# Kernel optimization log

Hardware: AMD Instinct MI355X
Metric: run time of the kernel (lower is better)

The kernel has to match this reference:

```python
import jax, jax.numpy as jnp
import numpy as np

D = 256          # node_embedding_dim (= GRU hidden per direction)
N = 1024         # number of frame nodes
C = 5            # num_classes
COUNTS = [15, 40, 15]   # num_intervals_per_scale
BINS = [80, 60, 80]     # dist_bins_list
MAX_T = 512      # fixed pad length for per-interval sequences (jit-static)


def _quant(w):
    # int8 per-tensor symmetric fake-quant with straight-through estimator
    s = jnp.maximum(jnp.max(jnp.abs(w)) / 127.0, 1e-8)
    q = jnp.clip(jnp.round(w / s), -128, 127) * s
    return w + jax.lax.stop_gradient(q - w)


def _gru_dir(x, eff, wih, whh, bih, bhh):
    # x: [I, T, D] packed-at-front sequences, eff: [I] valid lengths (>=1)
    # masked scan == torch packed GRU final hidden state
    I, T, _ = x.shape
    H = whh.shape[1]
    valid = jnp.arange(T)[None, :] < eff[:, None]   # [I, T]

    def step(h, inp):
        x_t, v = inp                                # [I,D], [I]
        gi = x_t @ wih.T + bih                      # [I, 3H]
        gh = h @ whh.T + bhh
        ir, iz, inn = jnp.split(gi, 3, axis=1)
        hr, hz, hn = jnp.split(gh, 3, axis=1)
        r = jax.nn.sigmoid(ir + hr)
        z = jax.nn.sigmoid(iz + hz)
        n = jnp.tanh(inn + r * hn)
        h = jnp.where(v[:, None], (1.0 - z) * n + z * h, h)
        return h, None

    h0 = jnp.zeros((I, H), x.dtype)
    hF, _ = jax.lax.scan(step, h0, (jnp.swapaxes(x, 0, 1), valid.T))
    return hF


def _forward(node_embeddings, time_positions, node_pred, audio_len, anchor_intervals,
             gru_wih, gru_whh, gru_bih, gru_bhh, w1, w2,
             w3_s0, w3_s1, w3_s2, sw_s0, ew_s0, sw_s1, ew_s1, sw_s2, ew_s2):
    al = audio_len[0]
    tpos = time_positions[:, 0] * al                     # [N]
    abn = jax.nn.softmax(node_pred, axis=-1)[:, 0]       # abnormal scores [N]
    w3s = [w3_s0, w3_s1, w3_s2]
    sws = [sw_s0, sw_s1, sw_s2]
    ews = [ew_s0, ew_s1, ew_s2]
    offs = np.concatenate([[0], np.cumsum(COUNTS)])
    bounds, confs, clss = [], [], []
    for si in range(3):
        I, b = COUNTS[si], BINS[si]
        anc = anchor_intervals[offs[si]:offs[si + 1]]    # [I, 2]
        starts, ends = anc[:, 0], anc[:, 1]
        # interval membership mask [I, N]
        mask = (tpos[None, :] >= starts[:, None]) & (tpos[None, :] <= ends[:, None])
        # compact valid nodes to the front (stable, preserves node order like x[mask])
        order = jnp.argsort(jnp.logical_not(mask), axis=1, stable=True)[:, :MAX_T]
        msort = jnp.take_along_axis(mask, order, axis=1)
        x_loc = node_embeddings[order] * msort[..., None]   # [I, MAX_T, D]; empty -> zeros row
        eff = jnp.clip(mask.sum(axis=1), 1, MAX_T)          # empty interval behaves as one zero step
        hf = _gru_dir(x_loc, eff, gru_wih[si, 0], gru_whh[si, 0], gru_bih[si, 0], gru_bhh[si, 0])
        # backward direction: reverse each valid prefix
        rev_idx = jnp.clip(eff[:, None] - 1 - jnp.arange(MAX_T)[None, :], 0, MAX_T - 1)
        x_rev = jnp.take_along_axis(x_loc, rev_idx[..., None], axis=1)
        hb = _gru_dir(x_rev, eff, gru_wih[si, 1], gru_whh[si, 1], gru_bih[si, 1], gru_bhh[si, 1])
        # shared feature: [2D | abnormal | center | width | 4 zero pads] = 2D+7
        feat = jnp.concatenate([
            hf, hb,
            abn[:I, None],
            ((starts + ends) * 0.5 / al)[:, None],
            ((ends - starts) / al)[:, None],
            jnp.zeros((I, 4), hf.dtype),
        ], axis=1)
        h = jax.nn.relu(feat @ _quant(w1[si]).T)   # dropout = identity (eval)
        h = jax.nn.relu(h @ _quant(w2[si]).T)
        out = h @ _quant(w3s[si]).T                # [I, 2b+1+(C-1)]
        so = jnp.sum(jax.nn.softmax(out[:, :b], axis=1) * sws[si], axis=1)
        eo = jnp.sum(jax.nn.softmax(out[:, b:2 * b], axis=1) * ews[si], axis=1)
        bounds.append(jnp.stack([jnp.clip(starts + so, 0.0, al), jnp.clip(ends + eo, 0.0, al)], axis=1))
        confs.append(out[:, 2 * b])
        clss.append(out[:, 2 * b + 1:])
    return (jnp.concatenate(bounds, axis=0),   # final_bounds [70, 2]
            jnp.concatenate(confs, axis=0),    # interval_conf_logits [70]
            jnp.concatenate(clss, axis=0))     # interval_cls_logits [70, 4]


def setup_inputs() -> dict:
    key = jax.random.key(0)
    ks = jax.random.split(key, 16)
    inp = {}
    inp["node_embeddings"] = jax.random.normal(ks[0], (N, D), jnp.float32)
    inp["time_positions"] = jax.random.uniform(ks[1], (N, 1), dtype=jnp.float32)
    inp["node_pred"] = jax.random.normal(ks[2], (N, C), jnp.float32)
    inp["audio_len"] = jnp.ones((1,), jnp.float32)
    rng = np.random.default_rng(0)
    widths = [0.05, 0.12, 0.30]
    rows = []
    for c, w in zip(COUNTS, widths):
        s = rng.uniform(0.0, 1.0 - w, size=c).astype(np.float32)
        e = s + rng.uniform(0.5 * w, w, size=c).astype(np.float32)
        rows.append(np.stack([s, e], axis=1))
    inp["anchor_intervals"] = jnp.asarray(np.concatenate(rows, axis=0))
    H = D
    def u(k, shape, fan):
        lim = 1.0 / np.sqrt(fan)
        return jax.random.uniform(k, shape, jnp.float32, -lim, lim)
    # GRU params stacked over [scale, direction]
    inp["gru_wih"] = u(ks[3], (3, 2, 3 * H, D), H)
    inp["gru_whh"] = u(ks[4], (3, 2, 3 * H, H), H)
    inp["gru_bih"] = u(ks[5], (3, 2, 3 * H), H)
    inp["gru_bhh"] = u(ks[6], (3, 2, 3 * H), H)
    F_in = 2 * D + 7
    inp["w1"] = u(ks[7], (3, 256, F_in), F_in)
    inp["w2"] = u(ks[8], (3, 256, 256), 256)
    inp["w3_s0"] = u(ks[9], (2 * BINS[0] + 1 + (C - 1), 256), 256)
    inp["w3_s1"] = u(ks[10], (2 * BINS[1] + 1 + (C - 1), 256), 256)
    inp["w3_s2"] = u(ks[11], (2 * BINS[2] + 1 + (C - 1), 256), 256)
    for i, nb in enumerate(BINS):
        inp[f"sw_s{i}"] = jnp.linspace(-20.0, 20.0, nb, dtype=jnp.float32)
        inp[f"ew_s{i}"] = jnp.linspace(-20.0, 20.0, nb, dtype=jnp.float32)
    return inp


def reference(node_embeddings, time_positions, node_pred, audio_len, anchor_intervals,
              gru_wih, gru_whh, gru_bih, gru_bhh, w1, w2,
              w3_s0, w3_s1, w3_s2, sw_s0, ew_s0, sw_s1, ew_s1, sw_s2, ew_s2):
    return _forward(node_embeddings, time_positions, node_pred, audio_len, anchor_intervals,
                    gru_wih, gru_whh, gru_bih, gru_bhh, w1, w2,
                    w3_s0, w3_s1, w3_s2, sw_s0, ew_s0, sw_s1, ew_s1, sw_s2, ew_s2)
```

## Files before the change

### kernel.cpp

```cpp
#include <hip/hip_runtime.h>
#include <math.h>

#define NN 1024
#define NNP 1025
#define DD 256
#define CC 5
#define G3 768
#define MAXT 512
#define NA 70

typedef _Float16 v8h __attribute__((ext_vector_type(8)));
typedef _Float16 v4h __attribute__((ext_vector_type(4)));
typedef float v4f __attribute__((ext_vector_type(4)));
typedef int v4i __attribute__((ext_vector_type(4)));

#define NF1 (3*16*17*64)
#define NF2 (3*16*8*64)
#define NF3 (3*11*8*64)
#define NFT (NF1+NF2+NF3)

__device__ __forceinline__ float sigf(float x){ return __fdividef(1.f, 1.f + __expf(-x)); }
__device__ __forceinline__ float tanhf_fast(float x){ return 1.f - __fdividef(2.f, __expf(2.f*x) + 1.f); }

__global__ __launch_bounds__(256) void mega_kernel(
    const float* __restrict__ node_pred, const float* __restrict__ tp_in,
    const float* __restrict__ audio_len, const float* __restrict__ anchors,
    const float* __restrict__ whh, const float* __restrict__ wih,
    const float* __restrict__ emb,
    const float* __restrict__ bih, const float* __restrict__ bhh,
    const float* __restrict__ w1, const float* __restrict__ w2,
    const float* __restrict__ w30, const float* __restrict__ w31, const float* __restrict__ w32,
    float* __restrict__ abn, int* __restrict__ order, int* __restrict__ cnteff,
    float* __restrict__ qs, float* __restrict__ cm,
    uint4* __restrict__ whhB8, _Float16* __restrict__ E){
  __shared__ __align__(16) unsigned char smem[16*264*2];
  int b = blockIdx.x, tid = threadIdx.x;
  if (b < 4){
    int i = b*256 + tid;
    float pv[CC]; float m = -1e30f;
    for (int c=0;c<CC;++c){ pv[c]=node_pred[i*CC+c]; m=fmaxf(m,pv[c]); }
    float s=0.f;
    for (int c=0;c<CC;++c) s += expf(pv[c]-m);
    abn[i] = expf(pv[0]-m)/s;
  } else if (b < 74){
    if (tid >= 64) return;
    int a = b-4; int lane = tid;
    float al = audio_len[0];
    float s = anchors[2*a], e = anchors[2*a+1];
    int* ord = order + a*MAXT;
    int cnt = 0;
    for (int base=0; base<NN; base+=64){
      float tp = tp_in[base+lane]*al;
      bool msk = (tp>=s)&&(tp<=e);
      unsigned long long bal = __ballot(msk);
      int off = (int)__popcll(bal & ((1ull<<lane)-1ull));
      if (msk && (cnt+off)<MAXT) ord[cnt+off] = base+lane;
      cnt += (int)__popcll(bal);
    }
    if (lane==0){ int c = cnt<MAXT?cnt:MAXT; cnteff[2*a]=c; cnteff[2*a+1]=(c>0)?c:1; }
  } else if (b < 83){
    int m = b-74;
    const float* p; int n;
    if (m<3){ p = w1 + (size_t)m*256*519; n = 256*519; }
    else if (m<6){ p = w2 + (size_t)(m-3)*256*256; n = 256*256; }
    else { p = (m==6)?w30:((m==7)?w31:w32); n = ((m==7)?125:165)*256; }
    float mx = 0.f;
    for (int i=tid;i<n;i+=256) mx = fmaxf(mx, fabsf(p[i]));
    float* red = (float*)smem;
    red[tid]=mx; __syncthreads();
    for (int sft=128; sft>0; sft>>=1){ if (tid<sft) red[tid]=fmaxf(red[tid],red[tid+sft]); __syncthreads(); }
    if (tid==0) qs[m] = fmaxf(red[0]/127.f, 1e-8f);
  } else if (b < 101){
    int i = (b-83)*256 + tid;
    if (i >= 4608) return;
    int gt = i % 3; int c = (i/3)&255; int sd = i/768;
    int j = gt*256 + c;
    float v = bih[sd*G3+j] + ((gt<2)? bhh[sd*G3+j] : 0.f);
    E[((size_t)(sd*NNP + NN))*1024 + c*4 + gt] = (_Float16)v;
  } else if (b < 149){
    int bb = b-101;
    int sd = bb>>3, w = bb&7;
    float* cm_lds = (float*)smem;
    int lane = tid & 63, wv = tid >> 6;
    for (int it=0; it<24; ++it){
      int lr = it*4 + wv;
      int gt = lr>>5, c = lr&31;
      int j = gt*256 + w*32 + c;
      float4 v = reinterpret_cast<const float4*>(whh + ((size_t)sd*G3 + j)*DD)[lane];
      float mx = fmaxf(fmaxf(fabsf(v.x),fabsf(v.y)), fmaxf(fabsf(v.z),fabsf(v.w)));
      #pragma unroll
      for (int sh=1; sh<64; sh<<=1) mx = fmaxf(mx, __shfl_xor(mx, sh));
      if (lane==0){
        float cmax = fmaxf(mx, 1e-12f);
        cm_lds[lr] = cmax;
        cm[sd*G3 + j] = cmax;
      }
    }
    __syncthreads();
    #pragma unroll
    for (int ee=0; ee<6; ++ee){
      int il = tid*6 + ee;
      int q    = il & 3;
      int nt   = (il>>2) % 6;
      int lane2= il / 24;
      int gt = nt>>1, half = nt&1;
      int j  = gt*256 + w*32 + half*16 + (lane2&15);
      int lr = gt*32  + half*16 + (lane2&15);
      int kbase = 64*q + 16*(lane2>>4);
      float inv = 127.f/cm_lds[lr];
      const float* src = whh + ((size_t)sd*G3 + j)*DD + kbase;
      unsigned int dw[4];
      #pragma unroll
      for (int d2=0; d2<4; ++d2){
        unsigned int acc = 0;
        #pragma unroll
        for (int e2=0; e2<4; ++e2){
          float qv = rintf(src[4*d2+e2]*inv);
          qv = fminf(fmaxf(qv,-127.f),127.f);
          int iq = (int)qv;
          acc |= ((unsigned int)(iq & 255)) << (8*e2);
        }
        dw[d2] = acc;
      }
      uint4 v; v.x=dw[0]; v.y=dw[1]; v.z=dw[2]; v.w=dw[3];
      whhB8[(size_t)(sd*8 + w)*1536 + il] = v;
    }
  } else {
    typedef _Float16 AsT[264];
    AsT* As = (AsT*)smem;
    int b2 = b - 149;
    int sd = b2 / 96;
    int rem = b2 - sd*96;
    int cg = rem >> 3, rq = rem & 7;
    int lane = tid & 63, wv = tid >> 6;
    int l15 = lane & 15, g16 = lane >> 4;
    int c_t = cg*4 + wv;
    int j = c_t*16 + l15;
    const float* Bp = wih + ((size_t)sd*G3 + j)*DD + 8*g16;
    float bsum = bih[sd*G3 + j] + (((j>>8) < 2) ? bhh[sd*G3 + j] : 0.f);
    v8h bf[8];
    #pragma unroll
    for (int q=0;q<8;++q){
      float4 b0 = *reinterpret_cast<const float4*>(Bp + 32*q);
      float4 b1 = *reinterpret_cast<const float4*>(Bp + 32*q + 4);
      v8h o;
      o[0]=(_Float16)b0.x; o[1]=(_Float16)b0.y; o[2]=(_Float16)b0.z; o[3]=(_Float16)b0.w;
      o[4]=(_Float16)b1.x; o[5]=(_Float16)b1.y; o[6]=(_Float16)b1.z; o[7]=(_Float16)b1.w;
      bf[q] = o;
    }
    int gt = j>>8, cc = j&255;
    for (int rt8=0; rt8<8; ++rt8){
      int row0 = (rq*8 + rt8)*16;
      {
        int rr = tid>>4, k0 = (tid&15)*16;
        const float4* ep = reinterpret_cast<const float4*>(emb + (size_t)(row0+rr)*DD + k0);
        #pragma unroll
        for (int f=0; f<4; ++f){
          float4 v = ep[f];
          v4h o; o[0]=(_Float16)v.x; o[1]=(_Float16)v.y; o[2]=(_Float16)v.z; o[3]=(_Float16)v.w;
          *reinterpret_cast<v4h*>(&As[rr][k0 + f*4]) = o;
        }
      }
      __syncthreads();
      v4f acc = {0.f,0.f,0.f,0.f};
      #pragma unroll
      for (int q=0;q<8;++q){
        v8h af = *reinterpret_cast<const v8h*>(&As[l15][32*q + 8*g16]);
        acc = __builtin_amdgcn_mfma_f32_16x16x32_f16(af, bf[q], acc, 0,0,0);
      }
      #pragma unroll
      for (int r=0;r<4;++r){
        int row = row0 + g16*4 + r;
        E[((size_t)(sd*NNP + row))*1024 + cc*4 + gt] = (_Float16)(acc[r] + bsum);
      }
      __syncthreads();
    }
  }
}

__global__ __launch_bounds__(512, 2) void gru_kernel(
    const _Float16* __restrict__ E, const v4i* __restrict__ whhB8,
    const float* __restrict__ bhh, const float* __restrict__ cm,
    const int* __restrict__ order, const int* __restrict__ cnteff,
    float* __restrict__ hout,
    const float* __restrict__ w1, const float* __restrict__ w2,
    const float* __restrict__ w30, const float* __restrict__ w31, const float* __restrict__ w32,
    const float* __restrict__ qs,
    v8h* __restrict__ w1F, v8h* __restrict__ w2F, v8h* __restrict__ w3F){
  int blk = blockIdx.x;
  int tid = threadIdx.x;
  if (blk >= NA*2){
    int i = (blk - NA*2)*512 + tid;
    if (i < NF1){
      int lane = i & 63; int rest = i >> 6;
      int q = rest % 17; int rc = rest / 17;
      int ct = rc & 15; int si = rc >> 4;
      int j = ct*16 + (lane&15);
      int k0 = q*32 + 8*(lane>>4);
      float inv = 1.f/qs[si];
      const float* src = w1 + ((size_t)(si*256 + j))*519;
      v8h o;
      #pragma unroll
      for (int e=0;e<8;++e){
        int k = k0+e;
        float wv = (k<519)? src[k] : 0.f;
        float qv = rintf(wv*inv);
        qv = fminf(fmaxf(qv,-128.f),127.f);
        o[e] = (_Float16)qv;
      }
      w1F[i] = o;
    } else if (i < NF1+NF2){
      int r = i - NF1;
      int lane = r & 63; int rest = r >> 6;
      int q = rest & 7; int rc = rest >> 3;
      int ct = rc & 15; int si = rc >> 4;
      int j = ct*16 + (lane&15);
      int k0 = q*32 + 8*(lane>>4);
      float inv = 1.f/qs[3+si];
      const float* src = w2 + ((size_t)(si*256 + j))*256 + k0;
      v8h o;
      #pragma unroll
      for (int e=0;e<8;++e){
        float qv = rintf(src[e]*inv);
        qv = fminf(fmaxf(qv,-128.f),127.f);
        o[e] = (_Float16)qv;
      }
      w2F[r] = o;
    } else if (i < NFT){
      int r = i - NF1 - NF2;
      int lane = r & 63; int rest = r >> 6;
      int q = rest & 7; int rc = rest >> 3;
      int ct = rc % 11; int si = rc / 11;
      int j = ct*16 + (lane&15);
      int nout = (si==1)?125:165;
      const float* w3 = (si==0)?w30:((si==1)?w31:w32);
      int k0 = q*32 + 8*(lane>>4);
      float inv = 1.f/qs[6+si];
      v8h o;
      #pragma unroll
      for (int e=0;e<8;++e){
        float wv = (j<nout)? w3[(size_t)j*256 + k0+e] : 0.f;
        float qv = rintf(wv*inv);
        qv = fminf(fmaxf(qv,-128.f),127.f);
        o[e] = (_Float16)qv;
      }
      w3F[r] = o;
    }
    return;
  }
  int a = blk>>1, d = blk&1;
  int si = (a<15)?0:((a<55)?1:2);
  int sd = si*2+d;
  int w = tid>>6, lane = tid&63;
  int g16 = lane>>4;
  int ct = g16 & 1;

  __shared__ int ord_s[MAXT];
  __shared__ alignas(16) signed char h8[2][DD];

  ord_s[tid] = order[a*MAXT + tid];
  if (tid < DD) h8[0][tid] = 0;

  int cnt = cnteff[2*a], eff = cnteff[2*a+1];

  int c = w*32 + (lane&31);
  float bn = bhh[sd*G3 + 2*DD + c];
  const float ISQ = 1.f/(127.f*127.f);
  float sr = cm[sd*G3 +        c]*ISQ;
  float sz = cm[sd*G3 + 256 +  c]*ISQ;
  float sn = cm[sd*G3 + 512 +  c]*ISQ;

  v4i bf[6][4];
  {
    const v4i* wp = whhB8 + (((size_t)sd*8 + w)*64 + lane)*24;
    #pragma unroll
    for (int nt=0;nt<6;++nt)
      #pragma unroll
      for (int q=0;q<4;++q)
        bf[nt][q] = wp[nt*4+q];
  }

  const uint2* Eb = reinterpret_cast<const uint2*>(E) + (size_t)sd*NNP*256;

  __syncthreads();

  float h = 0.f;
  uint2 gEven, gOdd;
  {
    int idx0 = d ? (eff-1) : 0;
    int n0 = (idx0 < cnt) ? ord_s[idx0] : NN;
    gEven = Eb[(size_t)n0*256 + c];
  }

  for (int t=0;t<eff;++t){
    int p = t & 1;
    if (t+1 < eff){
      int idx1 = d ? (eff-2-t) : (t+1);
      int n1 = (idx1 < cnt) ? ord_s[idx1] : NN;
      if (p==0) gOdd  = Eb[(size_t)n1*256 + c];
      else      gEven = Eb[(size_t)n1*256 + c];
    }
    v4i acc0={0,0,0,0}, acc1={0,0,0,0}, acc2={0,0,0,0};
    v4i acc3={0,0,0,0}, acc4={0,0,0,0}, acc5={0,0,0,0};
    #pragma unroll
    for (int q=0;q<4;++q){
      v4i af = *reinterpret_cast<const v4i*>(&h8[p][64*q + 16*g16]);
      acc0 = __builtin_amdgcn_mfma_i32_16x16x64_i8(af, bf[0][q], acc0, 0,0,0);
      acc1 = __builtin_amdgcn_mfma_i32_16x16x64_i8(af, bf[1][q], acc1, 0,0,0);
      acc2 = __builtin_amdgcn_mfma_i32_16x16x64_i8(af, bf[2][q], acc2, 0,0,0);
      acc3 = __builtin_amdgcn_mfma_i32_16x16x64_i8(af, bf[3][q], acc3, 0,0,0);
      acc4 = __builtin_amdgcn_mfma_i32_16x16x64_i8(af, bf[4][q], acc4, 0,0,0);
      acc5 = __builtin_amdgcn_mfma_i32_16x16x64_i8(af, bf[5][q], acc5, 0,0,0);
    }
    v4h ev = __builtin_bit_cast(v4h, (p==0) ? gEven : gOdd);
    int ir  = (ct==0) ? acc0[0] : acc1[0];
    int iz  = (ct==0) ? acc2[0] : acc3[0];
    int inn = (ct==0) ? acc4[0] : acc5[0];
    float r  = sigf((float)ev[0] + (float)ir*sr);
    float z  = sigf((float)ev[1] + (float)iz*sz);
    float nv = tanhf_fast((float)ev[2] + r*((float)inn*sn + bn));
    h = z*(h - nv) + nv;
    if (lane < 32) h8[p^1][c] = (signed char)(int)rintf(h*127.f);
    __syncthreads();
  }
  if (lane < 32) hout[(size_t)(2*a+d)*DD + c] = h;
}

__global__ __launch_bounds__(512) void mlp_kernel(
    const float* __restrict__ hout, const float* __restrict__ abn,
    const float* __restrict__ anchors, const float* __restrict__ audio_len,
    const v8h* __restrict__ w1F, const v8h* __restrict__ w2F, const v8h* __restrict__ w3F,
    const float* __restrict__ qs,
    const float* __restrict__ sw0, const float* __restrict__ ew0,
    const float* __restrict__ sw1, const float* __restrict__ ew1,
    const float* __restrict__ sw2, const float* __restrict__ ew2,
    float* __restrict__ out){
  int bm = blockIdx.x;
  int si = (bm==0)?0:((bm<4)?1:2);
  int mt = (bm==0)?0:((bm<4)?(bm-1):0);
  int cntA = (si==1)?40:15;
  int offA = (si==0)?0:((si==1)?15:55);
  int bb   = (si==1)?60:80;
  int m0 = mt*16;
  const float* sw = (si==0)?sw0:((si==1)?sw1:sw2);
  const float* ew = (si==0)?ew0:((si==1)?ew1:ew2);
  float al = audio_len[0];

  __shared__ _Float16 feat[16][552];
  __shared__ _Float16 h1s[16][264];
  __shared__ float    os[16][184];

  int tid = threadIdx.x;
  int lane = tid & 63, wv = tid >> 6;
  int l15 = lane & 15, g16 = lane >> 4;

  for (int idx = tid; idx < 16*552; idx += 512){
    int r = idx / 552, c2 = idx - r*552;
    float v = 0.f;
    int m = m0 + r;
    if (m < cntA){
      int a = offA + m;
      if (c2 < 256)       v = hout[(size_t)(2*a)*DD + c2];
      else if (c2 < 512)  v = hout[(size_t)(2*a+1)*DD + (c2-256)];
      else if (c2 == 512) v = abn[m];
      else if (c2 == 513){ float s=anchors[2*a], e=anchors[2*a+1]; v = (s+e)*0.5f/al; }
      else if (c2 == 514){ float s=anchors[2*a], e=anchors[2*a+1]; v = (e-s)/al; }
    }
    feat[r][c2] = (_Float16)v;
  }
  __syncthreads();
  float sc1 = qs[si], sc2 = qs[3+si], sc3 = qs[6+si];

  for (int nt = wv; nt < 16; nt += 8){
    int j = nt*16 + l15;
    const v8h* bp = w1F + (size_t)(si*16 + nt)*17*64 + lane;
    v4f acc = {0.f,0.f,0.f,0.f};
    for (int kq = 0; kq < 17; ++kq){
      v8h af = *reinterpret_cast<const v8h*>(&feat[l15][kq*32 + 8*g16]);
      acc = __builtin_amdgcn_mfma_f32_16x16x32_f16(af, bp[kq*64], acc, 0,0,0);
    }
    #pragma unroll
    for (int r=0;r<4;++r) h1s[g16*4+r][j] = (_Float16)fmaxf(acc[r]*sc1, 0.f);
  }
  __syncthreads();
  for (int nt = wv; nt < 16; nt += 8){
    int j = nt*16 + l15;
    const v8h* bp = w2F + (size_t)(si*16 + nt)*8*64 + lane;
    v4f acc = {0.f,0.f,0.f,0.f};
    for (int kq = 0; kq < 8; ++kq){
      v8h af = *reinterpret_cast<const v8h*>(&h1s[l15][kq*32 + 8*g16]);
      acc = __builtin_amdgcn_mfma_f32_16x16x32_f16(af, bp[kq*64], acc, 0,0,0);
    }
    #pragma unroll
    for (int r=0;r<4;++r) feat[g16*4+r][j] = (_Float16)fmaxf(acc[r]*sc2, 0.f);
  }
  __syncthreads();
  for (int nt = wv; nt < 11; nt += 8){
    int j = nt*16 + l15;
    const v8h* bp = w3F + (size_t)(si*11 + nt)*8*64 + lane;
    v4f acc = {0.f,0.f,0.f,0.f};
    for (int kq = 0; kq < 8; ++kq){
      v8h af = *reinterpret_cast<const v8h*>(&feat[l15][kq*32 + 8*g16]);
      acc = __builtin_amdgcn_mfma_f32_16x16x32_f16(af, bp[kq*64], acc, 0,0,0);
    }
    #pragma unroll
    for (int r=0;r<4;++r) os[g16*4+r][j] = acc[r]*sc3;
  }
  __syncthreads();
  for (int lm = wv; lm < 16; lm += 8){
    int m = m0 + lm;
    if (m >= cntA) continue;
    int a = offA + m;
    float s = anchors[2*a], e = anchors[2*a+1];
    float x0 = (lane < bb) ? os[lm][lane] : -1e30f;
    float x1 = (lane+64 < bb) ? os[lm][lane+64] : -1e30f;
    float mx = fmaxf(x0, x1);
    #pragma unroll
    for (int sh=1; sh<64; sh<<=1) mx = fmaxf(mx, __shfl_xor(mx, sh));
    float e0 = (lane < bb) ? expf(x0-mx) : 0.f;
    float e1 = (lane+64 < bb) ? expf(x1-mx) : 0.f;
    float se = e0 + e1;
    float ws2 = e0*((lane<bb)?sw[lane]:0.f) + e1*((lane+64<bb)?sw[lane+64]:0.f);
    #pragma unroll
    for (int sh=1; sh<64; sh<<=1){ se += __shfl_xor(se, sh); ws2 += __shfl_xor(ws2, sh); }
    float so = ws2/se;
    float y0 = (lane < bb) ? os[lm][bb+lane] : -1e30f;
    float y1 = (lane+64 < bb) ? os[lm][bb+lane+64] : -1e30f;
    float my = fmaxf(y0, y1);
    #pragma unroll
    for (int sh=1; sh<64; sh<<=1) my = fmaxf(my, __shfl_xor(my, sh));
    float f0 = (lane < bb) ? expf(y0-my) : 0.f;
    float f1 = (lane+64 < bb) ? expf(y1-my) : 0.f;
    float sf = f0 + f1;
    float wf = f0*((lane<bb)?ew[lane]:0.f) + f1*((lane+64<bb)?ew[lane+64]:0.f);
    #pragma unroll
    for (int sh=1; sh<64; sh<<=1){ sf += __shfl_xor(sf, sh); wf += __shfl_xor(wf, sh); }
    float eo = wf/sf;
    if (lane == 0){
      out[2*a]   = fminf(fmaxf(s+so, 0.f), al);
      out[2*a+1] = fminf(fmaxf(e+eo, 0.f), al);
      out[140+a] = os[lm][2*bb];
    }
    if (lane < 4) out[210+4*a+lane] = os[lm][2*bb+1+lane];
  }
}

extern "C" void kernel_launch(void* const* d_in, const int* in_sizes, int n_in,
                              void* d_out, int out_size, void* d_ws, size_t ws_size,
                              hipStream_t stream){
  const float* emb   = (const float*)d_in[0];
  const float* tpin  = (const float*)d_in[1];
  const float* npred = (const float*)d_in[2];
  const float* alen  = (const float*)d_in[3];
  const float* anch  = (const float*)d_in[4];
  const float* wih   = (const float*)d_in[5];
  const float* whh   = (const float*)d_in[6];
  const float* bih   = (const float*)d_in[7];
  const float* bhh   = (const float*)d_in[8];
  const float* w1    = (const float*)d_in[9];
  const float* w2    = (const float*)d_in[10];
  const float* w30   = (const float*)d_in[11];
  const float* w31   = (const float*)d_in[12];
  const float* w32   = (const float*)d_in[13];
  const float* sw0   = (const float*)d_in[14];
  const float* ew0   = (const float*)d_in[15];
  const float* sw1   = (const float*)d_in[16];
  const float* ew1   = (const float*)d_in[17];
  const float* sw2   = (const float*)d_in[18];
  const float* ew2   = (const float*)d_in[19];

  char* ws = (char*)d_ws;
  size_t off = 0;
  auto take = [&](size_t bytes)->char*{
    char* p = ws + off;
    off = (off + bytes + 255) & ~(size_t)255;
    return p;
  };
  float* abn    = (float*)take((size_t)NN*4);
  int*   order_ = (int*)  take((size_t)NA*MAXT*4);
  int*   cnteff = (int*)  take((size_t)NA*2*4);
  float* qs     = (float*)take(16*4);
  float* cm     = (float*)take((size_t)6*G3*4);
  uint4* whhB8  = (uint4*)take((size_t)6*8*1536*16);
  _Float16* E   = (_Float16*)take((size_t)6*NNP*1024*2);
  float* hout   = (float*)take((size_t)NA*2*DD*4);
  v8h* w1F      = (v8h*)take((size_t)NF1*16);
  v8h* w2F      = (v8h*)take((size_t)NF2*16);
  v8h* w3F      = (v8h*)take((size_t)NF3*16);
  (void)ws_size; (void)in_sizes; (void)n_in; (void)out_size;

  mega_kernel<<<dim3(725), dim3(256), 0, stream>>>(npred, tpin, alen, anch, whh, wih, emb,
                                                   bih, bhh, w1, w2, w30, w31, w32,
                                                   abn, order_, cnteff, qs, cm, whhB8, E);
  {
    const int packBlocks = (NFT + 511)/512;
    gru_kernel<<<dim3(NA*2 + packBlocks), dim3(512), 0, stream>>>(
        E, (const v4i*)whhB8, bhh, cm, order_, cnteff, hout,
        w1, w2, w30, w31, w32, qs, w1F, w2F, w3F);
  }
  mlp_kernel<<<dim3(5), dim3(512), 0, stream>>>(hout, abn, anch, alen, w1F, w2F, w3F, qs,
                                                sw0, ew0, sw1, ew1, sw2, ew2, (float*)d_out);
}
```

Baseline: 371.8 us.

## Batch 16 GRU intervals per block to fill the MFMA M dimension

The GRU kernel now groups up to 16 intervals of the same scale and direction into one block, using all 16 rows of the int8 MFMA tile instead of a single broadcast row. The launch drops from 140 recurrent blocks to 10. Each block loops to the longest sequence length in its group and masks finished rows. This cuts the total number of serial MFMA steps and the repeated weight loads, but each block now runs as long as its longest interval. It also uses more shared memory for per-row order tables and more registers for the per-row gathered inputs.

```diff
diff --git a/kernel.cpp b/kernel.cpp
--- a/kernel.cpp
+++ b/kernel.cpp
@@ -8,6 +8,7 @@
 #define G3 768
 #define MAXT 512
 #define NA 70
+#define NGRU 10
 
 typedef _Float16 v8h __attribute__((ext_vector_type(8)));
 typedef _Float16 v4h __attribute__((ext_vector_type(4)));
@@ -189,8 +190,8 @@
     v8h* __restrict__ w1F, v8h* __restrict__ w2F, v8h* __restrict__ w3F){
   int blk = blockIdx.x;
   int tid = threadIdx.x;
-  if (blk >= NA*2){
-    int i = (blk - NA*2)*512 + tid;
+  if (blk >= NGRU){
+    int i = (blk - NGRU)*512 + tid;
     if (i < NF1){
       int lane = i & 63; int rest = i >> 6;
       int q = rest % 17; int rc = rest / 17;
@@ -248,27 +249,40 @@
     }
     return;
   }
-  int a = blk>>1, d = blk&1;
-  int si = (a<15)?0:((a<55)?1:2);
+  int d = blk & 1, q5 = blk >> 1;
+  int si = (q5==0)?0:((q5<4)?1:2);
+  int g  = (q5==0)?0:((q5<4)?(q5-1):0);
   int sd = si*2+d;
+  int cntA = (si==1)?40:15;
+  int offA = (si==0)?0:((si==1)?15:55);
   int w = tid>>6, lane = tid&63;
-  int g16 = lane>>4;
-  int ct = g16 & 1;
-
-  __shared__ int ord_s[MAXT];
-  __shared__ alignas(16) signed char h8[2][DD];
-
-  ord_s[tid] = order[a*MAXT + tid];
-  if (tid < DD) h8[0][tid] = 0;
-
-  int cnt = cnteff[2*a], eff = cnteff[2*a+1];
-
-  int c = w*32 + (lane&31);
-  float bn = bhh[sd*G3 + 2*DD + c];
+  int g16 = lane>>4, l15 = lane&15;
+
+  __shared__ int ord_s[16][MAXT];
+  __shared__ alignas(16) signed char h8f[2][4096];
+  __shared__ int effs_l[16], cnts_l[16];
+
+  for (int k=0;k<16;++k){
+    int ii = k*512 + tid;
+    int row = ii >> 9, idxo = ii & 511;
+    int m = g*16 + row;
+    ord_s[row][idxo] = (m < cntA) ? order[(size_t)(offA + m)*MAXT + idxo] : NN;
+  }
+  if (tid < 16){
+    int m = g*16 + tid;
+    int act = (m < cntA);
+    int a = offA + m;
+    cnts_l[tid] = act ? cnteff[2*a]   : 0;
+    effs_l[tid] = act ? cnteff[2*a+1] : 0;
+  }
+  for (int k=tid; k<1024; k+=512) ((int*)h8f[0])[k] = 0;
+
+  int c0 = w*32 + l15, c1 = c0 + 16;
+  float bn0 = bhh[sd*G3 + 2*DD + c0], bn1 = bhh[sd*G3 + 2*DD + c1];
   const float ISQ = 1.f/(127.f*127.f);
-  float sr = cm[sd*G3 +        c]*ISQ;
-  float sz = cm[sd*G3 + 256 +  c]*ISQ;
-  float sn = cm[sd*G3 + 512 +  c]*ISQ;
+  float sr0 = cm[sd*G3 +       c0]*ISQ, sr1 = cm[sd*G3 +       c1]*ISQ;
+  float sz0 = cm[sd*G3 + 256 + c0]*ISQ, sz1 = cm[sd*G3 + 256 + c1]*ISQ;
+  float sn0 = cm[sd*G3 + 512 + c0]*ISQ, sn1 = cm[sd*G3 + 512 + c1]*ISQ;
 
   v4i bf[6][4];
   {
@@ -280,50 +294,99 @@
         bf[nt][q] = wp[nt*4+q];
   }
 
+  __syncthreads();
+
+  int eff[4], cnt[4];
+  #pragma unroll
+  for (int r=0;r<4;++r){ int row = g16*4+r; eff[r]=effs_l[row]; cnt[r]=cnts_l[row]; }
+  int maxeff = 0;
+  for (int m=0;m<16;++m) maxeff = max(maxeff, effs_l[m]);
+
   const uint2* Eb = reinterpret_cast<const uint2*>(E) + (size_t)sd*NNP*256;
 
-  __syncthreads();
-
-  float h = 0.f;
-  uint2 gEven, gOdd;
-  {
-    int idx0 = d ? (eff-1) : 0;
-    int n0 = (idx0 < cnt) ? ord_s[idx0] : NN;
-    gEven = Eb[(size_t)n0*256 + c];
-  }
-
-  for (int t=0;t<eff;++t){
-    int p = t & 1;
-    if (t+1 < eff){
-      int idx1 = d ? (eff-2-t) : (t+1);
-      int n1 = (idx1 < cnt) ? ord_s[idx1] : NN;
-      if (p==0) gOdd  = Eb[(size_t)n1*256 + c];
-      else      gEven = Eb[(size_t)n1*256 + c];
-    }
-    v4i acc0={0,0,0,0}, acc1={0,0,0,0}, acc2={0,0,0,0};
-    v4i acc3={0,0,0,0}, acc4={0,0,0,0}, acc5={0,0,0,0};
-    #pragma unroll
-    for (int q=0;q<4;++q){
-      v4i af = *reinterpret_cast<const v4i*>(&h8[p][64*q + 16*g16]);
-      acc0 = __builtin_amdgcn_mfma_i32_16x16x64_i8(af, bf[0][q], acc0, 0,0,0);
-      acc1 = __builtin_amdgcn_mfma_i32_16x16x64_i8(af, bf[1][q], acc1, 0,0,0);
-      acc2 = __builtin_amdgcn_mfma_i32_16x16x64_i8(af, bf[2][q], acc2, 0,0,0);
-      acc3 = __builtin_amdgcn_mfma_i32_16x16x64_i8(af, bf[3][q], acc3, 0,0,0);
-      acc4 = __builtin_amdgcn_mfma_i32_16x16x64_i8(af, bf[4][q], acc4, 0,0,0);
-      acc5 = __builtin_amdgcn_mfma_i32_16x16x64_i8(af, bf[5][q], acc5, 0,0,0);
-    }
-    v4h ev = __builtin_bit_cast(v4h, (p==0) ? gEven : gOdd);
-    int ir  = (ct==0) ? acc0[0] : acc1[0];
-    int iz  = (ct==0) ? acc2[0] : acc3[0];
-    int inn = (ct==0) ? acc4[0] : acc5[0];
-    float r  = sigf((float)ev[0] + (float)ir*sr);
-    float z  = sigf((float)ev[1] + (float)iz*sz);
-    float nv = tanhf_fast((float)ev[2] + r*((float)inn*sn + bn));
-    h = z*(h - nv) + nv;
-    if (lane < 32) h8[p^1][c] = (signed char)(int)rintf(h*127.f);
-    __syncthreads();
-  }
-  if (lane < 32) hout[(size_t)(2*a+d)*DD + c] = h;
+  float h[8];
+  #pragma unroll
+  for (int i=0;i<8;++i) h[i]=0.f;
+
+  uint2 gA[8], gB[8];
+  #pragma unroll
+  for (int r=0;r<4;++r){
+    int n = NN;
+    if (0 < eff[r]){
+      int idx = d ? (eff[r]-1) : 0;
+      n = (idx < cnt[r]) ? ord_s[g16*4+r][idx] : NN;
+    }
+    gA[2*r]   = Eb[(size_t)n*256 + c0];
+    gA[2*r+1] = Eb[(size_t)n*256 + c1];
+  }
+  #pragma unroll
+  for (int i=0;i<8;++i) gB[i] = gA[i];
+
+  int wbase = (w>>1)*1024 + (w&1)*512 + l15;
+
+#define GRU_STEP(T, HBIN, HBOUT, GCUR, GNXT)                                      \
+  {                                                                               \
+    if ((T)+1 < maxeff){                                                          \
+      _Pragma("unroll")                                                           \
+      for (int r=0;r<4;++r){                                                      \
+        int tn = (T)+1, n = NN;                                                   \
+        if (tn < eff[r]){                                                         \
+          int idx = d ? (eff[r]-1-tn) : tn;                                       \
+          n = (idx < cnt[r]) ? ord_s[g16*4+r][idx] : NN;                          \
+        }                                                                         \
+        GNXT[2*r]   = Eb[(size_t)n*256 + c0];                                     \
+        GNXT[2*r+1] = Eb[(size_t)n*256 + c1];                                     \
+      }                                                                           \
+    }                                                                             \
+    v4i acc0={0,0,0,0}, acc1={0,0,0,0}, acc2={0,0,0,0};                           \
+    v4i acc3={0,0,0,0}, acc4={0,0,0,0}, acc5={0,0,0,0};                           \
+    _Pragma("unroll")                                                             \
+    for (int q=0;q<4;++q){                                                        \
+      v4i af = *reinterpret_cast<const v4i*>(HBIN + q*1024 + lane*16);            \
+      acc0 = __builtin_amdgcn_mfma_i32_16x16x64_i8(af, bf[0][q], acc0, 0,0,0);    \
+      acc1 = __builtin_amdgcn_mfma_i32_16x16x64_i8(af, bf[1][q], acc1, 0,0,0);    \
+      acc2 = __builtin_amdgcn_mfma_i32_16x16x64_i8(af, bf[2][q], acc2, 0,0,0);    \
+      acc3 = __builtin_amdgcn_mfma_i32_16x16x64_i8(af, bf[3][q], acc3, 0,0,0);    \
+      acc4 = __builtin_amdgcn_mfma_i32_16x16x64_i8(af, bf[4][q], acc4, 0,0,0);    \
+      acc5 = __builtin_amdgcn_mfma_i32_16x16x64_i8(af, bf[5][q], acc5, 0,0,0);    \
+    }                                                                             \
+    _Pragma("unroll")                                                             \
+    for (int r=0;r<4;++r){                                                        \
+      v4h e0 = __builtin_bit_cast(v4h, GCUR[2*r]);                                \
+      v4h e1 = __builtin_bit_cast(v4h, GCUR[2*r+1]);                              \
+      bool upd = ((T) < eff[r]);                                                  \
+      float rr0 = sigf((float)e0[0] + (float)acc0[r]*sr0);                        \
+      float zz0 = sigf((float)e0[1] + (float)acc2[r]*sz0);                        \
+      float nv0 = tanhf_fast((float)e0[2] + rr0*((float)acc4[r]*sn0 + bn0));      \
+      float hn0 = zz0*(h[2*r]-nv0)+nv0;                                           \
+      h[2*r] = upd ? hn0 : h[2*r];                                                \
+      HBOUT[wbase + (g16*4+r)*16] = (signed char)(int)rintf(h[2*r]*127.f);        \
+      float rr1 = sigf((float)e1[0] + (float)acc1[r]*sr1);                        \
+      float zz1 = sigf((float)e1[1] + (float)acc3[r]*sz1);                        \
+      float nv1 = tanhf_fast((float)e1[2] + rr1*((float)acc5[r]*sn1 + bn1));      \
+      float hn1 = zz1*(h[2*r+1]-nv1)+nv1;                                         \
+      h[2*r+1] = upd ? hn1 : h[2*r+1];                                            \
+      HBOUT[wbase + 256 + (g16*4+r)*16] = (signed char)(int)rintf(h[2*r+1]*127.f);\
+    }                                                                             \
+    __syncthreads();                                                              \
+  }
+
+  for (int t2=0; t2<maxeff; t2+=2){
+    GRU_STEP(t2,   h8f[0], h8f[1], gA, gB)
+    if (t2+1 < maxeff)
+      GRU_STEP(t2+1, h8f[1], h8f[0], gB, gA)
+  }
+#undef GRU_STEP
+
+  #pragma unroll
+  for (int r=0;r<4;++r){
+    int m = g*16 + g16*4 + r;
+    if (m < cntA){
+      int a = offA + m;
+      hout[(size_t)(2*a+d)*DD + c0] = h[2*r];
+      hout[(size_t)(2*a+d)*DD + c1] = h[2*r+1];
+    }
+  }
 }
 
 __global__ __launch_bounds__(512) void mlp_kernel(
@@ -494,7 +557,7 @@
                                                    abn, order_, cnteff, qs, cm, whhB8, E);
   {
     const int packBlocks = (NFT + 511)/512;
-    gru_kernel<<<dim3(NA*2 + packBlocks), dim3(512), 0, stream>>>(
+    gru_kernel<<<dim3(NGRU + packBlocks), dim3(512), 0, stream>>>(
         E, (const v4i*)whhB8, bhh, cm, order_, cnteff, hout,
         w1, w2, w30, w31, w32, qs, w1F, w2F, w3F);
   }
```

Result: slower. 833.0 us (+124.1%).
